# Optimization experiments

Measured on AMD Instinct MI355X. Metric: run time of the kernel, lower is better.

Reference implementation:

```python
import jax, jax.numpy as jnp
import numpy as np

N, E = 50000, 1600000
IN_DIM, EMBED, OUT = 512, 128, 64


def setup_inputs() -> dict:
    key = jax.random.key(0)
    k = jax.random.split(key, 8)
    x = jax.random.normal(k[0], (N, IN_DIM), dtype=jnp.float32)
    edge_index = jax.random.randint(k[1], (2, E), 0, N, dtype=jnp.int32)
    W_dense = jax.random.normal(k[2], (EMBED, IN_DIM), dtype=jnp.float32) * 0.02
    b_dense = jnp.zeros((EMBED,), dtype=jnp.float32)
    W_gat = jax.random.normal(k[3], (OUT, EMBED), dtype=jnp.float32) * 0.05
    att_src = jax.random.normal(k[4], (OUT,), dtype=jnp.float32) * 0.1
    att_dst = jax.random.normal(k[5], (OUT,), dtype=jnp.float32) * 0.1
    b_gat = jnp.zeros((OUT,), dtype=jnp.float32)
    return {"x": x, "edge_index": edge_index, "W_dense": W_dense, "b_dense": b_dense,
            "W_gat": W_gat, "att_src": att_src, "att_dst": att_dst, "b_gat": b_gat}


def reference(x, edge_index, W_dense, b_dense, W_gat, att_src, att_dst, b_gat):
    # dense -> LeakyReLU(0.01) (nn.LeakyReLU default)
    h = jax.nn.leaky_relu(x @ W_dense.T + b_dense, negative_slope=0.01)  # [N, EMBED]
    n = h.shape[0]
    # GATConv (PyG, heads=1, add_self_loops=True, negative_slope=0.2)
    loops = jnp.arange(n, dtype=edge_index.dtype)
    src = jnp.concatenate([edge_index[0], loops])
    dst = jnp.concatenate([edge_index[1], loops])
    g = h @ W_gat.T  # [N, OUT]
    a_src = g @ att_src  # [N]
    a_dst = g @ att_dst  # [N]
    e = jax.nn.leaky_relu(a_src[src] + a_dst[dst], negative_slope=0.2)  # [E+N]
    # segment softmax over destination neighborhoods (self loops guarantee non-empty)
    m = jax.ops.segment_max(e, dst, num_segments=n)
    e = jnp.exp(e - m[dst])
    denom = jax.ops.segment_sum(e, dst, num_segments=n)
    alpha = e / denom[dst]
    out = jax.ops.segment_sum(g[src] * alpha[:, None], dst, num_segments=n) + b_gat
    # original returns ([embed_x], [embed_x]); we return the single embedding tensor
    return out
```

## Files before the change

### kernel.cpp

```cpp
#include <hip/hip_runtime.h>
#include <hip/hip_fp16.h>
#include <math.h>

#define IN_DIM 512
#define EMBED 128
#define OUT_DIM 64
#define NBPAD 256
#define SEGSH 12
#define CAP_LDS 10240

typedef __attribute__((ext_vector_type(8))) short bf16x8;
typedef __attribute__((ext_vector_type(4))) float f32x4;

__device__ __forceinline__ float lrelu(float v, float s) { return v > 0.f ? v : v * s; }

__device__ __forceinline__ float readlane_f(float v, int l) {
  return __int_as_float(__builtin_amdgcn_readlane(__float_as_int(v), l));
}

__device__ __forceinline__ unsigned short f2bf(float f) {
  unsigned int u = __float_as_uint(f);
  u += 0x7fff + ((u >> 16) & 1);
  return (unsigned short)(u >> 16);
}
__device__ __forceinline__ float bf2f(unsigned short h) {
  return __uint_as_float(((unsigned int)h) << 16);
}

__device__ __forceinline__ unsigned int cvt_pk_bf16(float a, float b) {
  unsigned int r;
  asm("v_cvt_pk_bf16_f32 %0, %1, %2" : "=v"(r) : "v"(a), "v"(b));
  return r;
}

__device__ __forceinline__ void gl_lds16(const void* g, void* l) {
  __builtin_amdgcn_global_load_lds(
      (const __attribute__((address_space(1))) unsigned int*)g,
      (__attribute__((address_space(3))) unsigned int*)l, 16, 0, 0);
}

__global__ __launch_bounds__(256) void split_w_kernel(
    const float* __restrict__ Wd, unsigned short* __restrict__ Wdh,
    unsigned short* __restrict__ Wdl, const float* __restrict__ Wg,
    unsigned short* __restrict__ Wgh, unsigned short* __restrict__ Wgl) {
  int i = (blockIdx.x * 256 + threadIdx.x) * 4;
  const float* W;
  unsigned short *Wh, *Wl;
  int base;
  if (i < EMBED * IN_DIM) {
    W = Wd; Wh = Wdh; Wl = Wdl; base = i;
  } else {
    base = i - EMBED * IN_DIM;
    if (base >= OUT_DIM * EMBED) return;
    W = Wg; Wh = Wgh; Wl = Wgl;
  }
  float4 v = *(const float4*)(W + base);
  unsigned int h0 = cvt_pk_bf16(v.x, v.y);
  unsigned int h1 = cvt_pk_bf16(v.z, v.w);
  float r0 = v.x - __uint_as_float(h0 << 16);
  float r1 = v.y - __uint_as_float(h0 & 0xffff0000u);
  float r2 = v.z - __uint_as_float(h1 << 16);
  float r3 = v.w - __uint_as_float(h1 & 0xffff0000u);
  unsigned int l0 = cvt_pk_bf16(r0, r1);
  unsigned int l1 = cvt_pk_bf16(r2, r3);
  *(uint2*)(Wh + base) = make_uint2(h0, h1);
  *(uint2*)(Wl + base) = make_uint2(l0, l1);
}

__global__ __launch_bounds__(256) void gemm1_mfma_kernel(
    const float* __restrict__ x, const unsigned short* __restrict__ Wdh,
    const unsigned short* __restrict__ Wdl, const float* __restrict__ bd,
    unsigned int* __restrict__ hp, int N) {
  __shared__ __align__(16) unsigned char Bhs[2][8192];
  __shared__ __align__(16) unsigned char Bls[2][8192];

  const int tid = threadIdx.x;
  const int lane = tid & 63;
  const int wid = tid >> 6;
  const int mblk = blockIdx.x * 128;
  const int quad = lane >> 4;
  const int l15 = lane & 15;

  const float* aptr[2];
#pragma unroll
  for (int mi = 0; mi < 2; ++mi) {
    int rg = mblk + wid * 32 + mi * 16 + l15;
    if (rg >= N) rg = N - 1;
    aptr[mi] = x + (size_t)rg * IN_DIM + quad * 8;
  }
  float4 tc[2][2];
  auto loadA = [&](int k0) {
#pragma unroll
    for (int mi = 0; mi < 2; ++mi) {
      tc[mi][0] = *(const float4*)(aptr[mi] + k0);
      tc[mi][1] = *(const float4*)(aptr[mi] + k0 + 4);
    }
  };

  const char* bsrcH[2];
  const char* bsrcL[2];
  int bdst[2];
#pragma unroll
  for (int i = 0; i < 2; ++i) {
    int chunk = i * 256 + tid;
    int row = chunk >> 2, ch = chunk & 3;
    int cs = ch ^ ((row >> 1) & 3);
    size_t srcoff = (size_t)row * (IN_DIM * 2) + (cs << 4);
    bsrcH[i] = (const char*)Wdh + srcoff;
    bsrcL[i] = (const char*)Wdl + srcoff;
    bdst[i] = chunk * 16;
  }
  auto stageB = [&](int buf, int k0) {
    const size_t kb = (size_t)k0 * 2;
#pragma unroll
    for (int i = 0; i < 2; ++i) {
      gl_lds16(bsrcH[i] + kb, Bhs[buf] + bdst[i]);
      gl_lds16(bsrcL[i] + kb, Bls[buf] + bdst[i]);
    }
  };

  int boff[8];
#pragma unroll
  for (int ni = 0; ni < 8; ++ni) {
    int row = ni * 16 + l15;
    boff[ni] = row * 64 + ((quad ^ ((row >> 1) & 3)) << 4);
  }

  f32x4 acc[2][8];
#pragma unroll
  for (int i = 0; i < 2; ++i)
#pragma unroll
    for (int j = 0; j < 8; ++j) acc[i][j] = (f32x4){0.f, 0.f, 0.f, 0.f};

  stageB(0, 0);
  loadA(0);
  __syncthreads();

#pragma unroll 2
  for (int s = 0; s < IN_DIM / 32; ++s) {
    const int buf = s & 1;
    if (s + 1 < IN_DIM / 32) stageB(buf ^ 1, (s + 1) * 32);

    bf16x8 AH[2], AL[2];
#pragma unroll
    for (int mi = 0; mi < 2; ++mi) {
      float av[8] = {tc[mi][0].x, tc[mi][0].y, tc[mi][0].z, tc[mi][0].w,
                     tc[mi][1].x, tc[mi][1].y, tc[mi][1].z, tc[mi][1].w};
      union { unsigned int u[4]; bf16x8 v; } H, L;
#pragma unroll
      for (int i = 0; i < 4; ++i) {
        unsigned int hpk = cvt_pk_bf16(av[2 * i], av[2 * i + 1]);
        float q0 = av[2 * i] - __uint_as_float(hpk << 16);
        float q1 = av[2 * i + 1] - __uint_as_float(hpk & 0xffff0000u);
        H.u[i] = hpk;
        L.u[i] = cvt_pk_bf16(q0, q1);
      }
      AH[mi] = H.v;
      AL[mi] = L.v;
    }
    if (s + 1 < IN_DIM / 32) loadA((s + 1) * 32);

#pragma unroll
    for (int hf = 0; hf < 2; ++hf) {
      bf16x8 BH[4], BL[4];
#pragma unroll
      for (int j = 0; j < 4; ++j) {
        BH[j] = *(const bf16x8*)(Bhs[buf] + boff[hf * 4 + j]);
        BL[j] = *(const bf16x8*)(Bls[buf] + boff[hf * 4 + j]);
      }
#pragma unroll
      for (int mi = 0; mi < 2; ++mi)
#pragma unroll
        for (int j = 0; j < 4; ++j) {
          int ni = hf * 4 + j;
          acc[mi][ni] = __builtin_amdgcn_mfma_f32_16x16x32_bf16(AH[mi], BH[j], acc[mi][ni], 0, 0, 0);
          acc[mi][ni] = __builtin_amdgcn_mfma_f32_16x16x32_bf16(AL[mi], BH[j], acc[mi][ni], 0, 0, 0);
          acc[mi][ni] = __builtin_amdgcn_mfma_f32_16x16x32_bf16(AH[mi], BL[j], acc[mi][ni], 0, 0, 0);
        }
    }
    __syncthreads();
  }

#pragma unroll
  for (int mi = 0; mi < 2; ++mi)
#pragma unroll
    for (int ni = 0; ni < 8; ++ni) {
      int n = ni * 16 + l15;
      float b = bd[n];
#pragma unroll
      for (int r = 0; r < 4; ++r) {
        int m = mblk + wid * 32 + mi * 16 + quad * 4 + r;
        float v = lrelu(acc[mi][ni][r] + b, 0.01f);
        unsigned short hi = f2bf(v);
        unsigned short lo = f2bf(v - bf2f(hi));
        if (m < N) hp[(size_t)m * EMBED + n] = ((unsigned int)hi << 16) | lo;
      }
    }
}

__global__ __launch_bounds__(256) void gemm2_mfma_kernel(
    const unsigned int* __restrict__ hp, const unsigned short* __restrict__ Wgh,
    const unsigned short* __restrict__ Wgl, const float* __restrict__ att_src,
    const float* __restrict__ att_dst, __half* __restrict__ gh,
    float* __restrict__ a_src, float* __restrict__ a_dst, int N) {
  __shared__ __align__(16) unsigned char Bhs[16384];
  __shared__ __align__(16) unsigned char Bls[16384];

  const int tid = threadIdx.x;
  const int lane = tid & 63;
  const int wid = tid >> 6;
  const int mblk = blockIdx.x * 128;
  const int quad = lane >> 4;
  const int l15 = lane & 15;

  const char* aptr[2];
#pragma unroll
  for (int mi = 0; mi < 2; ++mi) {
    int rg = mblk + wid * 32 + mi * 16 + l15;
    if (rg >= N) rg = N - 1;
    aptr[mi] = (const char*)hp + (size_t)rg * (EMBED * 4) + quad * 32;
  }
  uint4 areg[2][4][2];
#pragma unroll
  for (int mi = 0; mi < 2; ++mi)
#pragma unroll
    for (int ks = 0; ks < 4; ++ks) {
      areg[mi][ks][0] = *(const uint4*)(aptr[mi] + ks * 128);
      areg[mi][ks][1] = *(const uint4*)(aptr[mi] + ks * 128 + 16);
    }

#pragma unroll
  for (int i = 0; i < 4; ++i) {
    int chunk = i * 256 + tid;
    int row = chunk >> 4, ch = chunk & 15;
    size_t srcoff = (size_t)row * (EMBED * 2) + ((ch ^ (row & 15)) << 4);
    gl_lds16((const char*)Wgh + srcoff, Bhs + chunk * 16);
    gl_lds16((const char*)Wgl + srcoff, Bls + chunk * 16);
  }
  __syncthreads();

  f32x4 acc[2][4];
#pragma unroll
  for (int i = 0; i < 2; ++i)
#pragma unroll
    for (int j = 0; j < 4; ++j) acc[i][j] = (f32x4){0.f, 0.f, 0.f, 0.f};

#pragma unroll
  for (int ks = 0; ks < 4; ++ks) {
    bf16x8 AH[2], AL[2];
#pragma unroll
    for (int mi = 0; mi < 2; ++mi) {
      union { unsigned int u[8]; uint4 v[2]; } W_;
      W_.v[0] = areg[mi][ks][0];
      W_.v[1] = areg[mi][ks][1];
      union { unsigned int u[4]; bf16x8 v; } H, L;
#pragma unroll
      for (int p = 0; p < 4; ++p) {
        unsigned int wA = W_.u[2 * p], wB = W_.u[2 * p + 1];
        H.u[p] = __builtin_amdgcn_perm(wB, wA, 0x07060302u);
        L.u[p] = __builtin_amdgcn_perm(wB, wA, 0x05040100u);
      }
      AH[mi] = H.v;
      AL[mi] = L.v;
    }
#pragma unroll
    for (int ni = 0; ni < 4; ++ni) {
      int row = ni * 16 + l15;
      int chunk = ks * 4 + quad;
      int off = row * 256 + (((chunk ^ (row & 15))) << 4);
      bf16x8 BH = *(const bf16x8*)(Bhs + off);
      bf16x8 BL = *(const bf16x8*)(Bls + off);
#pragma unroll
      for (int mi = 0; mi < 2; ++mi) {
        acc[mi][ni] = __builtin_amdgcn_mfma_f32_16x16x32_bf16(AH[mi], BH, acc[mi][ni], 0, 0, 0);
        acc[mi][ni] = __builtin_amdgcn_mfma_f32_16x16x32_bf16(AL[mi], BH, acc[mi][ni], 0, 0, 0);
        acc[mi][ni] = __builtin_amdgcn_mfma_f32_16x16x32_bf16(AH[mi], BL, acc[mi][ni], 0, 0, 0);
      }
    }
  }

  float as_[4], ad_[4];
#pragma unroll
  for (int ni = 0; ni < 4; ++ni) {
    int n = ni * 16 + l15;
    as_[ni] = att_src[n];
    ad_[ni] = att_dst[n];
  }
#pragma unroll
  for (int mi = 0; mi < 2; ++mi) {
#pragma unroll
    for (int r = 0; r < 4; ++r) {
      int m = mblk + wid * 32 + mi * 16 + quad * 4 + r;
      float ps = acc[mi][0][r] * as_[0] + acc[mi][1][r] * as_[1] +
                 acc[mi][2][r] * as_[2] + acc[mi][3][r] * as_[3];
      float pd = acc[mi][0][r] * ad_[0] + acc[mi][1][r] * ad_[1] +
                 acc[mi][2][r] * ad_[2] + acc[mi][3][r] * ad_[3];
#pragma unroll
      for (int d = 1; d < 16; d <<= 1) {
        ps += __shfl_xor(ps, d, 64);
        pd += __shfl_xor(pd, d, 64);
      }
      if (m < N) {
#pragma unroll
        for (int ni = 0; ni < 4; ++ni)
          gh[(size_t)m * OUT_DIM + ni * 16 + l15] = __float2half(acc[mi][ni][r]);
        if (l15 == 0) {
          a_src[m] = ps;
          a_dst[m] = pd;
        }
      }
    }
  }
}

__global__ __launch_bounds__(256) void hist_count_kernel(
    const int* __restrict__ ei, int* __restrict__ histT, int nblkP, int E,
    int N) {
  __shared__ int cnt[NBPAD];
  const int t = threadIdx.x;
  cnt[t] = 0;
  __syncthreads();
  const int T = E + N;
  const int base = blockIdx.x << SEGSH;
#pragma unroll
  for (int q = 0; q < (1 << SEGSH) / 256; ++q) {
    int i = base + q * 256 + t;
    if (i < T) {
      int d = (i < E) ? ei[E + i] : (i - E);
      atomicAdd(&cnt[d >> 8], 1);
    }
  }
  __syncthreads();
  histT[(size_t)t * nblkP + blockIdx.x] = cnt[t];
}

__global__ __launch_bounds__(256) void row_scan_kernel(
    int* __restrict__ histT, int* __restrict__ bucket_tot, int nblkP) {
  __shared__ int sc[256];
  const int t = threadIdx.x;
  int* row = histT + (size_t)blockIdx.x * nblkP;
  const int per = (nblkP + 255) / 256;
  int loc[8];
  int sum = 0;
#pragma unroll 4
  for (int j = 0; j < per; ++j) {
    int idx = t * per + j;
    int v = (idx < nblkP) ? row[idx] : 0;
    loc[j] = sum;
    sum += v;
  }
  sc[t] = sum;
  __syncthreads();
  for (int dlt = 1; dlt < 256; dlt <<= 1) {
    int add = (t >= dlt) ? sc[t - dlt] : 0;
    __syncthreads();
    sc[t] += add;
    __syncthreads();
  }
  const int off = sc[t] - sum;
#pragma unroll 4
  for (int j = 0; j < per; ++j) {
    int idx = t * per + j;
    if (idx < nblkP) row[idx] = off + loc[j];
  }
  if (t == 255) bucket_tot[blockIdx.x] = sc[255];
}

__global__ __launch_bounds__(256) void base_scan_kernel(
    const int* __restrict__ bucket_tot, int* __restrict__ bucket_base,
    int* __restrict__ offsets, int N, int T) {
  __shared__ int sc[256];
  const int t = threadIdx.x;
  int v = bucket_tot[t];
  sc[t] = v;
  __syncthreads();
  for (int dlt = 1; dlt < 256; dlt <<= 1) {
    int add = (t >= dlt) ? sc[t - dlt] : 0;
    __syncthreads();
    sc[t] += add;
    __syncthreads();
  }
  bucket_base[t] = sc[t] - v;
  if (t == 0) offsets[N] = T;
}

__global__ __launch_bounds__(256) void bin_kernel(
    const int* __restrict__ ei, const int* __restrict__ histT,
    const int* __restrict__ bucket_base, int* __restrict__ stageB, int nblkP,
    int E, int N) {
  __shared__ int cnt[NBPAD];
  __shared__ int basev[NBPAD];
  const int t = threadIdx.x;
  cnt[t] = 0;
  basev[t] = bucket_base[t] + histT[(size_t)t * nblkP + blockIdx.x];
  __syncthreads();
  const int T = E + N;
  const int base = blockIdx.x << SEGSH;
#pragma unroll
  for (int q = 0; q < (1 << SEGSH) / 256; ++q) {
    int i = base + q * 256 + t;
    if (i < T) {
      int s, d;
      if (i < E) {
        s = ei[i];
        d = ei[E + i];
      } else {
        s = d = i - E;
      }
      int b = d >> 8;
      int r = atomicAdd(&cnt[b], 1);
      stageB[basev[b] + r] = (s << 8) | (d & 255);
    }
  }
}

__global__ __launch_bounds__(256) void build_kernel(
    const int* __restrict__ stageB, const int* __restrict__ bucket_base,
    const int* __restrict__ bucket_tot, const float* __restrict__ a_src,
    const float* __restrict__ a_dst, int* __restrict__ offsets,
    int2* __restrict__ csr_pack, int N) {
  __shared__ int cnt[256];
  __shared__ int pre[256];
  __shared__ int cur[256];
  __shared__ int2 buf[CAP_LDS];
  const int b = blockIdx.x;
  const int t = threadIdx.x;
  const int base = bucket_base[b];
  const int tot = bucket_tot[b];
  cnt[t] = 0;
  __syncthreads();
  const int* sp = stageB + base;
  for (int i = t; i < tot; i += 256) atomicAdd(&cnt[sp[i] & 255], 1);
  __syncthreads();
  int v = cnt[t];
  pre[t] = v;
  __syncthreads();
  for (int dlt = 1; dlt < 256; dlt <<= 1) {
    int add = (t >= dlt) ? pre[t - dlt] : 0;
    __syncthreads();
    pre[t] += add;
    __syncthreads();
  }
  const int excl = pre[t] - v;
  cur[t] = excl;
  const int d_self = (b << 8) | t;
  if (d_self < N) offsets[d_self] = base + excl;
  __syncthreads();
  for (int i = t; i < tot; i += 256) {
    int rec = sp[i];
    int dl = rec & 255;
    int s = rec >> 8;
    float e = a_src[s] + a_dst[(b << 8) | dl];
    e = e > 0.f ? e : 0.2f * e;
    int pos = atomicAdd(&cur[dl], 1);
    int2 r2 = make_int2(s, __float_as_int(e));
    if (pos < CAP_LDS)
      buf[pos] = r2;
    else
      csr_pack[base + pos] = r2;
  }
  __syncthreads();
  const int lim = min(tot, CAP_LDS);
  for (int i = t; i < lim; i += 256) csr_pack[base + i] = buf[i];
}

__global__ __launch_bounds__(256) void aggregate_kernel(
    const int* __restrict__ offsets, const int2* __restrict__ csr_pack,
    const __half* __restrict__ gh, const float* __restrict__ b_gat,
    float* __restrict__ out, int N) {
  const int lane = threadIdx.x & 63;
  const int node = blockIdx.x * 4 + (threadIdx.x >> 6);
  if (node >= N) return;
  const int beg = offsets[node], end = offsets[node + 1];

  float m = -1e30f, l = 0.f;
  for (int j = beg + lane; j < end; j += 64) {
    float e = __int_as_float(csr_pack[j].y);
    if (e > m) {
      l = l * __expf(m - e) + 1.f;
      m = e;
    } else {
      l += __expf(e - m);
    }
  }
#pragma unroll
  for (int d = 1; d < 64; d <<= 1) {
    float mo = __shfl_xor(m, d, 64);
    float lo = __shfl_xor(l, d, 64);
    float M = fmaxf(m, mo);
    l = l * __expf(m - M) + lo * __expf(mo - M);
    m = M;
  }
  const float inv_l = 1.f / l;

  float acc0 = 0.f, acc1 = 0.f, acc2 = 0.f, acc3 = 0.f;
  for (int jb = beg; jb < end; jb += 64) {
    int j = jb + lane;
    float p = 0.f;
    int s = 0;
    if (j < end) {
      int2 rec = csr_pack[j];
      p = __expf(__int_as_float(rec.y) - m) * inv_l;
      s = rec.x;
    }
    const int cnt = min(64, end - jb);
    int jj = 0;
    for (; jj + 4 <= cnt; jj += 4) {
      int s0 = __builtin_amdgcn_readlane(s, jj);
      int s1 = __builtin_amdgcn_readlane(s, jj + 1);
      int s2 = __builtin_amdgcn_readlane(s, jj + 2);
      int s3 = __builtin_amdgcn_readlane(s, jj + 3);
      float p0 = readlane_f(p, jj);
      float p1 = readlane_f(p, jj + 1);
      float p2 = readlane_f(p, jj + 2);
      float p3 = readlane_f(p, jj + 3);
      acc0 += p0 * __half2float(gh[((size_t)s0 << 6) + lane]);
      acc1 += p1 * __half2float(gh[((size_t)s1 << 6) + lane]);
      acc2 += p2 * __half2float(gh[((size_t)s2 << 6) + lane]);
      acc3 += p3 * __half2float(gh[((size_t)s3 << 6) + lane]);
    }
    for (; jj < cnt; ++jj) {
      int s0 = __builtin_amdgcn_readlane(s, jj);
      float p0 = readlane_f(p, jj);
      acc0 += p0 * __half2float(gh[((size_t)s0 << 6) + lane]);
    }
  }
  out[(size_t)node * OUT_DIM + lane] = (acc0 + acc1) + (acc2 + acc3) + b_gat[lane];
}

extern "C" void kernel_launch(void* const* d_in, const int* in_sizes, int n_in,
                              void* d_out, int out_size, void* d_ws, size_t ws_size,
                              hipStream_t stream) {
  const float* x = (const float*)d_in[0];
  const int* ei = (const int*)d_in[1];
  const float* Wd = (const float*)d_in[2];
  const float* bd = (const float*)d_in[3];
  const float* Wg = (const float*)d_in[4];
  const float* att_src = (const float*)d_in[5];
  const float* att_dst = (const float*)d_in[6];
  const float* bg = (const float*)d_in[7];
  float* out = (float*)d_out;

  const int N = in_sizes[0] / IN_DIM;
  const int E = in_sizes[1] / 2;
  const int T = E + N;
  const int NB = (N + 255) >> 8;
  const int nblkP = (T + (1 << SEGSH) - 1) >> SEGSH;

  char* ws = (char*)d_ws;
  size_t off = 0;
  auto alloc = [&](size_t bytes) -> void* {
    void* p = ws + off;
    off += (bytes + 15) & ~(size_t)15;
    return p;
  };
  unsigned int* hpk = (unsigned int*)alloc((size_t)N * EMBED * 4);
  __half* gh = (__half*)alloc((size_t)N * OUT_DIM * 2);
  float* a_src = (float*)alloc((size_t)N * 4);
  float* a_dst = (float*)alloc((size_t)N * 4);
  int* offsets = (int*)alloc((size_t)(N + 1) * 4);
  int* histT = (int*)alloc((size_t)NBPAD * nblkP * 4);
  int* bucket_base = (int*)alloc((size_t)NBPAD * 4);
  int* bucket_tot = (int*)alloc((size_t)NBPAD * 4);
  int* stageB = (int*)alloc((size_t)T * 4);
  int2* csr_pack = (int2*)alloc((size_t)T * 8);
  unsigned short* Wdh = (unsigned short*)alloc((size_t)EMBED * IN_DIM * 2);
  unsigned short* Wdl = (unsigned short*)alloc((size_t)EMBED * IN_DIM * 2);
  unsigned short* Wgh = (unsigned short*)alloc((size_t)OUT_DIM * EMBED * 2);
  unsigned short* Wgl = (unsigned short*)alloc((size_t)OUT_DIM * EMBED * 2);

  const int SPLIT_TOT = EMBED * IN_DIM + OUT_DIM * EMBED;
  hipLaunchKernelGGL(split_w_kernel, dim3(SPLIT_TOT / 1024), dim3(256), 0,
                     stream, Wd, Wdh, Wdl, Wg, Wgh, Wgl);
  hipLaunchKernelGGL(gemm1_mfma_kernel, dim3((N + 127) / 128), dim3(256), 0,
                     stream, x, Wdh, Wdl, bd, hpk, N);
  hipLaunchKernelGGL(gemm2_mfma_kernel, dim3((N + 127) / 128), dim3(256), 0,
                     stream, hpk, Wgh, Wgl, att_src, att_dst, gh, a_src, a_dst, N);
  hipLaunchKernelGGL(hist_count_kernel, dim3(nblkP), dim3(256), 0, stream,
                     ei, histT, nblkP, E, N);
  hipLaunchKernelGGL(row_scan_kernel, dim3(NBPAD), dim3(256), 0, stream,
                     histT, bucket_tot, nblkP);
  hipLaunchKernelGGL(base_scan_kernel, dim3(1), dim3(256), 0, stream,
                     bucket_tot, bucket_base, offsets, N, T);
  hipLaunchKernelGGL(bin_kernel, dim3(nblkP), dim3(256), 0, stream,
                     ei, histT, bucket_base, stageB, nblkP, E, N);
  hipLaunchKernelGGL(build_kernel, dim3(NB), dim3(256), 0, stream,
                     stageB, bucket_base, bucket_tot, a_src, a_dst, offsets,
                     csr_pack, N);
  hipLaunchKernelGGL(aggregate_kernel, dim3((N + 3) / 4), dim3(256), 0, stream,
                     offsets, csr_pack, gh, bg, out, N);
}
```

Baseline: 306.2 us.

## Precompute softmax max, exponentials and inverse sums in CSR build kernel

```diff
diff --git a/kernel.cpp b/kernel.cpp
--- a/kernel.cpp
+++ b/kernel.cpp
@@ -7,7 +7,7 @@
 #define OUT_DIM 64
 #define NBPAD 256
 #define SEGSH 12
-#define CAP_LDS 10240
+#define CAP_LDS 12288
 
 typedef __attribute__((ext_vector_type(8))) short bf16x8;
 typedef __attribute__((ext_vector_type(4))) float f32x4;
@@ -25,6 +25,15 @@
 }
 __device__ __forceinline__ float bf2f(unsigned short h) {
   return __uint_as_float(((unsigned int)h) << 16);
+}
+
+__device__ __forceinline__ unsigned int fkey(float f) {
+  unsigned int b = __float_as_uint(f);
+  return b ^ ((unsigned int)((int)b >> 31) | 0x80000000u);
+}
+__device__ __forceinline__ float funkey(unsigned int k) {
+  unsigned int b = k ^ ((k & 0x80000000u) ? 0x80000000u : 0xFFFFFFFFu);
+  return __uint_as_float(b);
 }
 
 __device__ __forceinline__ unsigned int cvt_pk_bf16(float a, float b) {
@@ -418,16 +427,21 @@
     const int* __restrict__ stageB, const int* __restrict__ bucket_base,
     const int* __restrict__ bucket_tot, const float* __restrict__ a_src,
     const float* __restrict__ a_dst, int* __restrict__ offsets,
-    int2* __restrict__ csr_pack, int N) {
+    int2* __restrict__ csr_pack, float* __restrict__ linv, int N) {
   __shared__ int cnt[256];
   __shared__ int pre[256];
   __shared__ int cur[256];
+  __shared__ unsigned int mmax[256];
+  __shared__ float lsum[256];
   __shared__ int2 buf[CAP_LDS];
+  __shared__ unsigned char dlb[CAP_LDS];
   const int b = blockIdx.x;
   const int t = threadIdx.x;
   const int base = bucket_base[b];
   const int tot = bucket_tot[b];
   cnt[t] = 0;
+  mmax[t] = 0u;
+  lsum[t] = 0.f;
   __syncthreads();
   const int* sp = stageB + base;
   for (int i = t; i < tot; i += 256) atomicAdd(&cnt[sp[i] & 255], 1);
@@ -452,46 +466,38 @@
     int s = rec >> 8;
     float e = a_src[s] + a_dst[(b << 8) | dl];
     e = e > 0.f ? e : 0.2f * e;
+    atomicMax(&mmax[dl], fkey(e));
     int pos = atomicAdd(&cur[dl], 1);
     int2 r2 = make_int2(s, __float_as_int(e));
-    if (pos < CAP_LDS)
+    if (pos < CAP_LDS) {
       buf[pos] = r2;
-    else
+      dlb[pos] = (unsigned char)dl;
+    } else {
       csr_pack[base + pos] = r2;
+    }
   }
   __syncthreads();
   const int lim = min(tot, CAP_LDS);
+  for (int i = t; i < lim; i += 256) {
+    int dl = dlb[i];
+    float m = funkey(mmax[dl]);
+    float p = __expf(__int_as_float(buf[i].y) - m);
+    buf[i].y = __float_as_int(p);
+    atomicAdd(&lsum[dl], p);
+  }
+  __syncthreads();
+  if (d_self < N) linv[d_self] = 1.f / lsum[t];
   for (int i = t; i < lim; i += 256) csr_pack[base + i] = buf[i];
 }
 
 __global__ __launch_bounds__(256) void aggregate_kernel(
     const int* __restrict__ offsets, const int2* __restrict__ csr_pack,
-    const __half* __restrict__ gh, const float* __restrict__ b_gat,
-    float* __restrict__ out, int N) {
+    const __half* __restrict__ gh, const float* __restrict__ linv,
+    const float* __restrict__ b_gat, float* __restrict__ out, int N) {
   const int lane = threadIdx.x & 63;
   const int node = blockIdx.x * 4 + (threadIdx.x >> 6);
   if (node >= N) return;
   const int beg = offsets[node], end = offsets[node + 1];
-
-  float m = -1e30f, l = 0.f;
-  for (int j = beg + lane; j < end; j += 64) {
-    float e = __int_as_float(csr_pack[j].y);
-    if (e > m) {
-      l = l * __expf(m - e) + 1.f;
-      m = e;
-    } else {
-      l += __expf(e - m);
-    }
-  }
-#pragma unroll
-  for (int d = 1; d < 64; d <<= 1) {
-    float mo = __shfl_xor(m, d, 64);
-    float lo = __shfl_xor(l, d, 64);
-    float M = fmaxf(m, mo);
-    l = l * __expf(m - M) + lo * __expf(mo - M);
-    m = M;
-  }
-  const float inv_l = 1.f / l;
 
   float acc0 = 0.f, acc1 = 0.f, acc2 = 0.f, acc3 = 0.f;
   for (int jb = beg; jb < end; jb += 64) {
@@ -500,7 +506,7 @@
     int s = 0;
     if (j < end) {
       int2 rec = csr_pack[j];
-      p = __expf(__int_as_float(rec.y) - m) * inv_l;
+      p = __int_as_float(rec.y);
       s = rec.x;
     }
     const int cnt = min(64, end - jb);
@@ -525,7 +531,8 @@
       acc0 += p0 * __half2float(gh[((size_t)s0 << 6) + lane]);
     }
   }
-  out[(size_t)node * OUT_DIM + lane] = (acc0 + acc1) + (acc2 + acc3) + b_gat[lane];
+  out[(size_t)node * OUT_DIM + lane] =
+      ((acc0 + acc1) + (acc2 + acc3)) * linv[node] + b_gat[lane];
 }
 
 extern "C" void kernel_launch(void* const* d_in, const int* in_sizes, int n_in,
@@ -558,6 +565,7 @@
   __half* gh = (__half*)alloc((size_t)N * OUT_DIM * 2);
   float* a_src = (float*)alloc((size_t)N * 4);
   float* a_dst = (float*)alloc((size_t)N * 4);
+  float* linv = (float*)alloc((size_t)N * 4);
   int* offsets = (int*)alloc((size_t)(N + 1) * 4);
   int* histT = (int*)alloc((size_t)NBPAD * nblkP * 4);
   int* bucket_base = (int*)alloc((size_t)NBPAD * 4);
@@ -586,7 +594,7 @@
                      ei, histT, bucket_base, stageB, nblkP, E, N);
   hipLaunchKernelGGL(build_kernel, dim3(NB), dim3(256), 0, stream,
                      stageB, bucket_base, bucket_tot, a_src, a_dst, offsets,
-                     csr_pack, N);
+                     csr_pack, linv, N);
   hipLaunchKernelGGL(aggregate_kernel, dim3((N + 3) / 4), dim3(256), 0, stream,
-                     offsets, csr_pack, gh, bg, out, N);
-}
+                     offsets, csr_pack, gh, linv, bg, out, N);
+}
```

Result: slower. 319.0 us (+4.2%).

## Fuse dense GEMM and GAT projection GEMM into one kernel via LDS transpose

Applied to the files above, without the earlier changes.

```diff
diff --git a/kernel.cpp b/kernel.cpp
--- a/kernel.cpp
+++ b/kernel.cpp
@@ -67,12 +67,14 @@
   *(uint2*)(Wl + base) = make_uint2(l0, l1);
 }
 
-__global__ __launch_bounds__(256) void gemm1_mfma_kernel(
+__global__ __launch_bounds__(256) void gemm12_fused_kernel(
     const float* __restrict__ x, const unsigned short* __restrict__ Wdh,
     const unsigned short* __restrict__ Wdl, const float* __restrict__ bd,
-    unsigned int* __restrict__ hp, int N) {
-  __shared__ __align__(16) unsigned char Bhs[2][8192];
-  __shared__ __align__(16) unsigned char Bls[2][8192];
+    const unsigned short* __restrict__ Wgh, const unsigned short* __restrict__ Wgl,
+    const float* __restrict__ att_src, const float* __restrict__ att_dst,
+    __half* __restrict__ gh, float* __restrict__ a_src,
+    float* __restrict__ a_dst, int N) {
+  __shared__ __align__(16) unsigned char SMEM[65536];
 
   const int tid = threadIdx.x;
   const int lane = tid & 63;
@@ -114,8 +116,8 @@
     const size_t kb = (size_t)k0 * 2;
 #pragma unroll
     for (int i = 0; i < 2; ++i) {
-      gl_lds16(bsrcH[i] + kb, Bhs[buf] + bdst[i]);
-      gl_lds16(bsrcL[i] + kb, Bls[buf] + bdst[i]);
+      gl_lds16(bsrcH[i] + kb, SMEM + buf * 8192 + bdst[i]);
+      gl_lds16(bsrcL[i] + kb, SMEM + 16384 + buf * 8192 + bdst[i]);
     }
   };
 
@@ -132,6 +134,14 @@
 #pragma unroll
     for (int j = 0; j < 8; ++j) acc[i][j] = (f32x4){0.f, 0.f, 0.f, 0.f};
 
+#pragma unroll
+  for (int i = 0; i < 4; ++i) {
+    int chunk = i * 256 + tid;
+    int row = chunk >> 4, ch = chunk & 15;
+    size_t srcoff = (size_t)row * (EMBED * 2) + ((ch ^ (row & 15)) << 4);
+    gl_lds16((const char*)Wgh + srcoff, SMEM + 32768 + chunk * 16);
+    gl_lds16((const char*)Wgl + srcoff, SMEM + 49152 + chunk * 16);
+  }
   stageB(0, 0);
   loadA(0);
   __syncthreads();
@@ -165,8 +175,8 @@
       bf16x8 BH[4], BL[4];
 #pragma unroll
       for (int j = 0; j < 4; ++j) {
-        BH[j] = *(const bf16x8*)(Bhs[buf] + boff[hf * 4 + j]);
-        BL[j] = *(const bf16x8*)(Bls[buf] + boff[hf * 4 + j]);
+        BH[j] = *(const bf16x8*)(SMEM + buf * 8192 + boff[hf * 4 + j]);
+        BL[j] = *(const bf16x8*)(SMEM + 16384 + buf * 8192 + boff[hf * 4 + j]);
       }
 #pragma unroll
       for (int mi = 0; mi < 2; ++mi)
@@ -181,78 +191,46 @@
     __syncthreads();
   }
 
-#pragma unroll
-  for (int mi = 0; mi < 2; ++mi)
+  unsigned char* Tr = SMEM;
+  const unsigned char* WgHs = SMEM + 32768;
+  const unsigned char* WgLs = SMEM + 49152;
+
+  f32x4 acc2[2][4];
+#pragma unroll
+  for (int i = 0; i < 2; ++i)
+#pragma unroll
+    for (int j = 0; j < 4; ++j) acc2[i][j] = (f32x4){0.f, 0.f, 0.f, 0.f};
+
+#pragma unroll
+  for (int mi = 0; mi < 2; ++mi) {
+    __syncthreads();
 #pragma unroll
     for (int ni = 0; ni < 8; ++ni) {
       int n = ni * 16 + l15;
       float b = bd[n];
 #pragma unroll
       for (int r = 0; r < 4; ++r) {
-        int m = mblk + wid * 32 + mi * 16 + quad * 4 + r;
         float v = lrelu(acc[mi][ni][r] + b, 0.01f);
         unsigned short hi = f2bf(v);
         unsigned short lo = f2bf(v - bf2f(hi));
-        if (m < N) hp[(size_t)m * EMBED + n] = ((unsigned int)hi << 16) | lo;
-      }
-    }
-}
-
-__global__ __launch_bounds__(256) void gemm2_mfma_kernel(
-    const unsigned int* __restrict__ hp, const unsigned short* __restrict__ Wgh,
-    const unsigned short* __restrict__ Wgl, const float* __restrict__ att_src,
-    const float* __restrict__ att_dst, __half* __restrict__ gh,
-    float* __restrict__ a_src, float* __restrict__ a_dst, int N) {
-  __shared__ __align__(16) unsigned char Bhs[16384];
-  __shared__ __align__(16) unsigned char Bls[16384];
-
-  const int tid = threadIdx.x;
-  const int lane = tid & 63;
-  const int wid = tid >> 6;
-  const int mblk = blockIdx.x * 128;
-  const int quad = lane >> 4;
-  const int l15 = lane & 15;
-
-  const char* aptr[2];
-#pragma unroll
-  for (int mi = 0; mi < 2; ++mi) {
-    int rg = mblk + wid * 32 + mi * 16 + l15;
-    if (rg >= N) rg = N - 1;
-    aptr[mi] = (const char*)hp + (size_t)rg * (EMBED * 4) + quad * 32;
-  }
-  uint4 areg[2][4][2];
-#pragma unroll
-  for (int mi = 0; mi < 2; ++mi)
+        unsigned int pw = ((unsigned int)hi << 16) | lo;
+        int row16 = quad * 4 + r;
+        int col = ni * 16 + l15;
+        int cc = col >> 2;
+        int cs = cc ^ (row16 & 7);
+        *(unsigned int*)(Tr + wid * 8192 + row16 * 512 + cs * 16 +
+                         (col & 3) * 4) = pw;
+      }
+    }
+    __syncthreads();
 #pragma unroll
     for (int ks = 0; ks < 4; ++ks) {
-      areg[mi][ks][0] = *(const uint4*)(aptr[mi] + ks * 128);
-      areg[mi][ks][1] = *(const uint4*)(aptr[mi] + ks * 128 + 16);
-    }
-
-#pragma unroll
-  for (int i = 0; i < 4; ++i) {
-    int chunk = i * 256 + tid;
-    int row = chunk >> 4, ch = chunk & 15;
-    size_t srcoff = (size_t)row * (EMBED * 2) + ((ch ^ (row & 15)) << 4);
-    gl_lds16((const char*)Wgh + srcoff, Bhs + chunk * 16);
-    gl_lds16((const char*)Wgl + srcoff, Bls + chunk * 16);
-  }
-  __syncthreads();
-
-  f32x4 acc[2][4];
-#pragma unroll
-  for (int i = 0; i < 2; ++i)
-#pragma unroll
-    for (int j = 0; j < 4; ++j) acc[i][j] = (f32x4){0.f, 0.f, 0.f, 0.f};
-
-#pragma unroll
-  for (int ks = 0; ks < 4; ++ks) {
-    bf16x8 AH[2], AL[2];
-#pragma unroll
-    for (int mi = 0; mi < 2; ++mi) {
+      const int s7 = l15 & 7;
+      const int cc0 = ks * 8 + quad * 2;
+      const unsigned char* tb = Tr + wid * 8192 + l15 * 512;
       union { unsigned int u[8]; uint4 v[2]; } W_;
-      W_.v[0] = areg[mi][ks][0];
-      W_.v[1] = areg[mi][ks][1];
+      W_.v[0] = *(const uint4*)(tb + ((cc0 ^ s7) << 4));
+      W_.v[1] = *(const uint4*)(tb + (((cc0 + 1) ^ s7) << 4));
       union { unsigned int u[4]; bf16x8 v; } H, L;
 #pragma unroll
       for (int p = 0; p < 4; ++p) {
@@ -260,21 +238,17 @@
         H.u[p] = __builtin_amdgcn_perm(wB, wA, 0x07060302u);
         L.u[p] = __builtin_amdgcn_perm(wB, wA, 0x05040100u);
       }
-      AH[mi] = H.v;
-      AL[mi] = L.v;
-    }
-#pragma unroll
-    for (int ni = 0; ni < 4; ++ni) {
-      int row = ni * 16 + l15;
-      int chunk = ks * 4 + quad;
-      int off = row * 256 + (((chunk ^ (row & 15))) << 4);
-      bf16x8 BH = *(const bf16x8*)(Bhs + off);
-      bf16x8 BL = *(const bf16x8*)(Bls + off);
-#pragma unroll
-      for (int mi = 0; mi < 2; ++mi) {
-        acc[mi][ni] = __builtin_amdgcn_mfma_f32_16x16x32_bf16(AH[mi], BH, acc[mi][ni], 0, 0, 0);
-        acc[mi][ni] = __builtin_amdgcn_mfma_f32_16x16x32_bf16(AL[mi], BH, acc[mi][ni], 0, 0, 0);
-        acc[mi][ni] = __builtin_amdgcn_mfma_f32_16x16x32_bf16(AH[mi], BL, acc[mi][ni], 0, 0, 0);
+      bf16x8 AH2 = H.v, AL2 = L.v;
+#pragma unroll
+      for (int ni = 0; ni < 4; ++ni) {
+        int row = ni * 16 + l15;
+        int chunk = ks * 4 + quad;
+        int off = row * 256 + (((chunk ^ (row & 15))) << 4);
+        bf16x8 BH = *(const bf16x8*)(WgHs + off);
+        bf16x8 BL = *(const bf16x8*)(WgLs + off);
+        acc2[mi][ni] = __builtin_amdgcn_mfma_f32_16x16x32_bf16(AH2, BH, acc2[mi][ni], 0, 0, 0);
+        acc2[mi][ni] = __builtin_amdgcn_mfma_f32_16x16x32_bf16(AL2, BH, acc2[mi][ni], 0, 0, 0);
+        acc2[mi][ni] = __builtin_amdgcn_mfma_f32_16x16x32_bf16(AH2, BL, acc2[mi][ni], 0, 0, 0);
       }
     }
   }
@@ -291,10 +265,10 @@
 #pragma unroll
     for (int r = 0; r < 4; ++r) {
       int m = mblk + wid * 32 + mi * 16 + quad * 4 + r;
-      float ps = acc[mi][0][r] * as_[0] + acc[mi][1][r] * as_[1] +
-                 acc[mi][2][r] * as_[2] + acc[mi][3][r] * as_[3];
-      float pd = acc[mi][0][r] * ad_[0] + acc[mi][1][r] * ad_[1] +
-                 acc[mi][2][r] * ad_[2] + acc[mi][3][r] * ad_[3];
+      float ps = acc2[mi][0][r] * as_[0] + acc2[mi][1][r] * as_[1] +
+                 acc2[mi][2][r] * as_[2] + acc2[mi][3][r] * as_[3];
+      float pd = acc2[mi][0][r] * ad_[0] + acc2[mi][1][r] * ad_[1] +
+                 acc2[mi][2][r] * ad_[2] + acc2[mi][3][r] * ad_[3];
 #pragma unroll
       for (int d = 1; d < 16; d <<= 1) {
         ps += __shfl_xor(ps, d, 64);
@@ -303,7 +277,7 @@
       if (m < N) {
 #pragma unroll
         for (int ni = 0; ni < 4; ++ni)
-          gh[(size_t)m * OUT_DIM + ni * 16 + l15] = __float2half(acc[mi][ni][r]);
+          gh[(size_t)m * OUT_DIM + ni * 16 + l15] = __float2half(acc2[mi][ni][r]);
         if (l15 == 0) {
           a_src[m] = ps;
           a_dst[m] = pd;
@@ -554,7 +528,6 @@
     off += (bytes + 15) & ~(size_t)15;
     return p;
   };
-  unsigned int* hpk = (unsigned int*)alloc((size_t)N * EMBED * 4);
   __half* gh = (__half*)alloc((size_t)N * OUT_DIM * 2);
   float* a_src = (float*)alloc((size_t)N * 4);
   float* a_dst = (float*)alloc((size_t)N * 4);
@@ -572,10 +545,9 @@
   const int SPLIT_TOT = EMBED * IN_DIM + OUT_DIM * EMBED;
   hipLaunchKernelGGL(split_w_kernel, dim3(SPLIT_TOT / 1024), dim3(256), 0,
                      stream, Wd, Wdh, Wdl, Wg, Wgh, Wgl);
-  hipLaunchKernelGGL(gemm1_mfma_kernel, dim3((N + 127) / 128), dim3(256), 0,
-                     stream, x, Wdh, Wdl, bd, hpk, N);
-  hipLaunchKernelGGL(gemm2_mfma_kernel, dim3((N + 127) / 128), dim3(256), 0,
-                     stream, hpk, Wgh, Wgl, att_src, att_dst, gh, a_src, a_dst, N);
+  hipLaunchKernelGGL(gemm12_fused_kernel, dim3((N + 127) / 128), dim3(256), 0,
+                     stream, x, Wdh, Wdl, bd, Wgh, Wgl, att_src, att_dst,
+                     gh, a_src, a_dst, N);
   hipLaunchKernelGGL(hist_count_kernel, dim3(nblkP), dim3(256), 0, stream,
                      ei, histT, nblkP, E, N);
   hipLaunchKernelGGL(row_scan_kernel, dim3(NBPAD), dim3(256), 0, stream,
```

Result: faster. 295.9 us (-3.4%).
